# Optimization experiments

Measured on AMD Instinct MI355X. Metric: run time of the kernel, lower is better.

Reference implementation:

```python
import jax, jax.numpy as jnp
import numpy as np

COMMITMENT_COST = 0.25

def setup_inputs() -> dict:
    key = jax.random.key(0)
    k1, k2 = jax.random.split(key)
    inputs = jax.random.normal(k1, (32, 64, 64, 64), dtype=jnp.float32)  # [B, C=D, H, W]
    K, D = 512, 64
    # torch init: uniform(-1/K, 1/K)
    weight = jax.random.uniform(k2, (K, D), dtype=jnp.float32, minval=-1.0 / K, maxval=1.0 / K)
    return {"inputs": inputs, "weight": weight}

def reference(inputs, weight):
    B, C, H, W = inputs.shape
    x = jnp.transpose(inputs, (0, 2, 3, 1))  # [B, H, W, C]
    flat = x.reshape(-1, C)  # [N, D]
    # squared euclidean distances [N, K]
    d = (jnp.sum(flat ** 2, axis=1, keepdims=True)
         + jnp.sum(weight ** 2, axis=1)
         - 2.0 * flat @ weight.T)
    idx = jnp.argmin(d, axis=1)  # [N]
    quantized = weight[idx]  # gather == one-hot @ weight, [N, D]
    e_latent_loss = jnp.mean((jax.lax.stop_gradient(quantized) - flat) ** 2)
    q_latent_loss = jnp.mean((quantized - jax.lax.stop_gradient(flat)) ** 2)
    loss = q_latent_loss + COMMITMENT_COST * e_latent_loss
    # straight-through estimator
    q_st = flat + jax.lax.stop_gradient(quantized - flat)
    out = jnp.transpose(q_st.reshape(B, H, W, C), (0, 3, 1, 2))  # back to NCHW
    return out, loss
```

## Files before the change

### kernel.cpp

```cpp
#include <hip/hip_runtime.h>

typedef __attribute__((ext_vector_type(8))) __bf16 bf16x8;
typedef __attribute__((ext_vector_type(4))) float floatx4;

__device__ __forceinline__ unsigned short f2bf(float f) {
    unsigned int u = __builtin_bit_cast(unsigned int, f);
    unsigned int r = u + 0x7FFFu + ((u >> 16) & 1u);
    return (unsigned short)(r >> 16);
}

__global__ void vq_prep(const float* __restrict__ w, unsigned short* __restrict__ wbf,
                        float* __restrict__ wsq) {
    const int t = threadIdx.x;
    const int row = blockIdx.x * 4 + (t >> 6);
    const int c = t & 63;
    float v = w[row * 64 + c];
    wbf[row * 64 + c] = f2bf(v);
    float s = v * v;
#pragma unroll
    for (int off = 32; off; off >>= 1) s += __shfl_xor(s, off, 64);
    if (c == 0) wsq[row] = s;
}

__global__ void __launch_bounds__(256) vq_main(
    const float* __restrict__ in,
    const float* __restrict__ w,
    const unsigned short* __restrict__ wbf,
    const float* __restrict__ wsq,
    float* __restrict__ out,
    float* __restrict__ partials) {
    __shared__ unsigned short xs[8 * 64 * 8];
    __shared__ float wsqs[512];
    __shared__ float red_s[4][64];
    __shared__ int   red_i[4][64];
    __shared__ int   idx_final[64];
    __shared__ float wave_sum[4];

    const int t = threadIdx.x;
    const int lane = t & 63;
    const int wv = t >> 6;
    const int b = blockIdx.x >> 6;
    const int s0 = (blockIdx.x & 63) << 6;

    const float* in_base = in + ((size_t)b * 64) * 4096 + s0;

    wsqs[t] = wsq[t];
    wsqs[t + 256] = wsq[t + 256];

    const int jj = (t & 15) * 4;
    const int c0 = t >> 4;
#pragma unroll
    for (int co = 0; co < 64; co += 16) {
        const int c = co + c0;
        floatx4 v = *(const floatx4*)(in_base + (size_t)c * 4096 + jj);
        const int g = c >> 3, e = c & 7;
        unsigned short* p = &xs[((g * 64 + jj) * 8) + e];
        p[0]  = f2bf(v[0]);
        p[8]  = f2bf(v[1]);
        p[16] = f2bf(v[2]);
        p[24] = f2bf(v[3]);
    }
    __syncthreads();

    bf16x8 Bf[4][2];
    {
        const int half = lane >> 4;
        const int mcol = lane & 15;
#pragma unroll
        for (int mt = 0; mt < 4; ++mt) {
            const int m = mt * 16 + mcol;
#pragma unroll
            for (int h = 0; h < 2; ++h) {
                const int g = h * 4 + half;
                Bf[mt][h] = *(const bf16x8*)&xs[(g * 64 + m) * 8];
            }
        }
    }

    float best_s[4];
    int   best_i[4];
#pragma unroll
    for (int mt = 0; mt < 4; ++mt) { best_s[mt] = 1e30f; best_i[mt] = 0; }

    const int code_row = lane & 15;
    const int kgrp = lane >> 4;
#pragma unroll
    for (int cti = 0; cti < 8; ++cti) {
        const int ct = wv * 8 + cti;
        const int code_base = ct * 16;
        const unsigned short* arow = wbf + (code_base + code_row) * 64 + kgrp * 8;
        bf16x8 A0 = *(const bf16x8*)(arow);
        bf16x8 A1 = *(const bf16x8*)(arow + 32);
        floatx4 wq = *(const floatx4*)&wsqs[code_base + kgrp * 4];
#pragma unroll
        for (int mt = 0; mt < 4; ++mt) {
            floatx4 acc = {0.f, 0.f, 0.f, 0.f};
            acc = __builtin_amdgcn_mfma_f32_16x16x32_bf16(A0, Bf[mt][0], acc, 0, 0, 0);
            acc = __builtin_amdgcn_mfma_f32_16x16x32_bf16(A1, Bf[mt][1], acc, 0, 0, 0);
#pragma unroll
            for (int r = 0; r < 4; ++r) {
                const float sc = wq[r] - 2.f * acc[r];
                const int code = code_base + kgrp * 4 + r;
                if (sc < best_s[mt]) { best_s[mt] = sc; best_i[mt] = code; }
            }
        }
    }

#pragma unroll
    for (int mt = 0; mt < 4; ++mt) {
        float s = best_s[mt];
        int   i = best_i[mt];
#pragma unroll
        for (int d = 16; d < 64; d <<= 1) {
            const float s2 = __shfl_xor(s, d, 64);
            const int   i2 = __shfl_xor(i, d, 64);
            if (s2 < s || (s2 == s && i2 < i)) { s = s2; i = i2; }
        }
        if (lane < 16) { red_s[wv][mt * 16 + lane] = s; red_i[wv][mt * 16 + lane] = i; }
    }
    __syncthreads();
    if (t < 64) {
        float s = red_s[0][t];
        int   i = red_i[0][t];
#pragma unroll
        for (int w2 = 1; w2 < 4; ++w2) {
            const float s2 = red_s[w2][t];
            const int   i2 = red_i[w2][t];
            if (s2 < s || (s2 == s && i2 < i)) { s = s2; i = i2; }
        }
        idx_final[t] = i;
    }
    __syncthreads();

    int idxr[4];
    idxr[0] = idx_final[jj + 0];
    idxr[1] = idx_final[jj + 1];
    idxr[2] = idx_final[jj + 2];
    idxr[3] = idx_final[jj + 3];

    float lsum = 0.f;
    float* out_base = out + ((size_t)b * 64) * 4096 + s0;
#pragma unroll
    for (int co = 0; co < 64; co += 16) {
        const int c = co + c0;
        floatx4 xv = *(const floatx4*)(in_base + (size_t)c * 4096 + jj);
        floatx4 qv;
#pragma unroll
        for (int r = 0; r < 4; ++r) {
            const float wr = w[idxr[r] * 64 + c];
            qv[r] = wr;
            const float d = wr - xv[r];
            lsum += d * d;
        }
        *(floatx4*)(out_base + (size_t)c * 4096 + jj) = qv;
    }

#pragma unroll
    for (int off = 32; off; off >>= 1) lsum += __shfl_xor(lsum, off, 64);
    if (lane == 0) wave_sum[wv] = lsum;
    __syncthreads();
    if (t == 0) {
        partials[blockIdx.x] = wave_sum[0] + wave_sum[1] + wave_sum[2] + wave_sum[3];
    }
}

__global__ void vq_reduce(const float* __restrict__ partials, float* __restrict__ loss) {
    const int t = threadIdx.x;
    float s = 0.f;
#pragma unroll
    for (int i = 0; i < 8; ++i) s += partials[t + i * 256];
#pragma unroll
    for (int off = 32; off; off >>= 1) s += __shfl_xor(s, off, 64);
    __shared__ float ws4[4];
    if ((t & 63) == 0) ws4[t >> 6] = s;
    __syncthreads();
    if (t == 0) loss[0] = (ws4[0] + ws4[1] + ws4[2] + ws4[3]) * (1.25f / 8388608.f);
}

extern "C" void kernel_launch(void* const* d_in, const int* in_sizes, int n_in,
                              void* d_out, int out_size, void* d_ws, size_t ws_size,
                              hipStream_t stream) {
    const float* in = (const float*)d_in[0];
    const float* w  = (const float*)d_in[1];
    float* out = (float*)d_out;
    float* loss = out + 8388608;
    unsigned short* wbf = (unsigned short*)d_ws;
    float* wsq = (float*)((char*)d_ws + 512 * 64 * 2);
    float* partials = (float*)((char*)d_ws + 512 * 64 * 2 + 2048);

    vq_prep<<<128, 256, 0, stream>>>(w, wbf, wsq);
    vq_main<<<2048, 256, 0, stream>>>(in, w, wbf, wsq, out, partials);
    vq_reduce<<<1, 256, 0, stream>>>(partials, loss);
}
```

Before: 116.4 us.

## Restructure VQ kernel to single-wave blocks with 32x32 MFMA and packed argmin

```diff
diff --git a/kernel.cpp b/kernel.cpp
--- a/kernel.cpp
+++ b/kernel.cpp
@@ -2,6 +2,7 @@
 
 typedef __attribute__((ext_vector_type(8))) __bf16 bf16x8;
 typedef __attribute__((ext_vector_type(4))) float floatx4;
+typedef __attribute__((ext_vector_type(16))) float floatx16;
 
 __device__ __forceinline__ unsigned short f2bf(float f) {
     unsigned int u = __builtin_bit_cast(unsigned int, f);
@@ -22,39 +23,32 @@
     if (c == 0) wsq[row] = s;
 }
 
-__global__ void __launch_bounds__(256) vq_main(
+__global__ void __launch_bounds__(64, 4) vq_main(
     const float* __restrict__ in,
     const float* __restrict__ w,
     const unsigned short* __restrict__ wbf,
     const float* __restrict__ wsq,
     float* __restrict__ out,
     float* __restrict__ partials) {
-    __shared__ unsigned short xs[8 * 64 * 8];
-    __shared__ float wsqs[512];
-    __shared__ float red_s[4][64];
-    __shared__ int   red_i[4][64];
-    __shared__ int   idx_final[64];
-    __shared__ float wave_sum[4];
+    __shared__ unsigned short xs[8 * 32 * 8];
 
-    const int t = threadIdx.x;
-    const int lane = t & 63;
-    const int wv = t >> 6;
-    const int b = blockIdx.x >> 6;
-    const int s0 = (blockIdx.x & 63) << 6;
+    const int lane = threadIdx.x;
+    const int bid = blockIdx.x;
+    const int b = bid >> 7;
+    const int s0 = (bid & 127) << 5;
 
     const float* in_base = in + ((size_t)b * 64) * 4096 + s0;
+    const int c0 = lane >> 3;
+    const int jj = (lane & 7) * 4;
 
-    wsqs[t] = wsq[t];
-    wsqs[t + 256] = wsq[t + 256];
-
-    const int jj = (t & 15) * 4;
-    const int c0 = t >> 4;
+    float x2 = 0.f;
 #pragma unroll
-    for (int co = 0; co < 64; co += 16) {
-        const int c = co + c0;
-        floatx4 v = *(const floatx4*)(in_base + (size_t)c * 4096 + jj);
-        const int g = c >> 3, e = c & 7;
-        unsigned short* p = &xs[((g * 64 + jj) * 8) + e];
+    for (int co = 0; co < 64; co += 8) {
+        const int k = co + c0;
+        floatx4 v = *(const floatx4*)(in_base + (size_t)k * 4096 + jj);
+        x2 += v[0] * v[0] + v[1] * v[1] + v[2] * v[2] + v[3] * v[3];
+        const int g = k >> 3, e = k & 7;
+        unsigned short* p = &xs[(g * 32 + jj) * 8 + e];
         p[0]  = f2bf(v[0]);
         p[8]  = f2bf(v[1]);
         p[16] = f2bf(v[2]);
@@ -62,105 +56,68 @@
     }
     __syncthreads();
 
-    bf16x8 Bf[4][2];
-    {
-        const int half = lane >> 4;
-        const int mcol = lane & 15;
+    const int hi = lane >> 5;
+    const int col = lane & 31;
+
+    bf16x8 Bf[4];
 #pragma unroll
-        for (int mt = 0; mt < 4; ++mt) {
-            const int m = mt * 16 + mcol;
+    for (int ch = 0; ch < 4; ++ch) {
+        const int g = 2 * ch + hi;
+        Bf[ch] = *(const bf16x8*)&xs[(g * 32 + col) * 8];
+    }
+
+    float best = 1e30f;
+#pragma unroll 2
+    for (int ct = 0; ct < 16; ++ct) {
+        const int code_base = ct * 32;
+        const unsigned short* arow = wbf + (code_base + col) * 64 + hi * 8;
+        bf16x8 A0 = *(const bf16x8*)(arow);
+        bf16x8 A1 = *(const bf16x8*)(arow + 16);
+        bf16x8 A2 = *(const bf16x8*)(arow + 32);
+        bf16x8 A3 = *(const bf16x8*)(arow + 48);
+        floatx16 acc = {0.f, 0.f, 0.f, 0.f, 0.f, 0.f, 0.f, 0.f,
+                        0.f, 0.f, 0.f, 0.f, 0.f, 0.f, 0.f, 0.f};
+        acc = __builtin_amdgcn_mfma_f32_32x32x16_bf16(A0, Bf[0], acc, 0, 0, 0);
+        acc = __builtin_amdgcn_mfma_f32_32x32x16_bf16(A1, Bf[1], acc, 0, 0, 0);
+        acc = __builtin_amdgcn_mfma_f32_32x32x16_bf16(A2, Bf[2], acc, 0, 0, 0);
+        acc = __builtin_amdgcn_mfma_f32_32x32x16_bf16(A3, Bf[3], acc, 0, 0, 0);
 #pragma unroll
-            for (int h = 0; h < 2; ++h) {
-                const int g = h * 4 + half;
-                Bf[mt][h] = *(const bf16x8*)&xs[(g * 64 + m) * 8];
+        for (int q = 0; q < 4; ++q) {
+            floatx4 wq = *(const floatx4*)&wsq[code_base + 8 * q + 4 * hi];
+#pragma unroll
+            for (int rr = 0; rr < 4; ++rr) {
+                const int r = q * 4 + rr;
+                const float sc = __builtin_fmaf(-2.f, acc[r], wq[rr]);
+                const unsigned int code = (unsigned int)(code_base + 8 * q + 4 * hi + rr);
+                const unsigned int ub =
+                    (__builtin_bit_cast(unsigned int, sc) & 0xFFFFFE00u) | code;
+                best = fminf(best, __builtin_bit_cast(float, ub));
             }
         }
     }
+    best = fminf(best, __shfl_xor(best, 32, 64));
 
-    float best_s[4];
-    int   best_i[4];
+    const float smin =
+        __builtin_bit_cast(float, __builtin_bit_cast(unsigned int, best) & 0xFFFFFE00u);
+    float tot = x2 + (lane < 32 ? smin : 0.f);
 #pragma unroll
-    for (int mt = 0; mt < 4; ++mt) { best_s[mt] = 1e30f; best_i[mt] = 0; }
-
-    const int code_row = lane & 15;
-    const int kgrp = lane >> 4;
-#pragma unroll
-    for (int cti = 0; cti < 8; ++cti) {
-        const int ct = wv * 8 + cti;
-        const int code_base = ct * 16;
-        const unsigned short* arow = wbf + (code_base + code_row) * 64 + kgrp * 8;
-        bf16x8 A0 = *(const bf16x8*)(arow);
-        bf16x8 A1 = *(const bf16x8*)(arow + 32);
-        floatx4 wq = *(const floatx4*)&wsqs[code_base + kgrp * 4];
-#pragma unroll
-        for (int mt = 0; mt < 4; ++mt) {
-            floatx4 acc = {0.f, 0.f, 0.f, 0.f};
-            acc = __builtin_amdgcn_mfma_f32_16x16x32_bf16(A0, Bf[mt][0], acc, 0, 0, 0);
-            acc = __builtin_amdgcn_mfma_f32_16x16x32_bf16(A1, Bf[mt][1], acc, 0, 0, 0);
-#pragma unroll
-            for (int r = 0; r < 4; ++r) {
-                const float sc = wq[r] - 2.f * acc[r];
-                const int code = code_base + kgrp * 4 + r;
-                if (sc < best_s[mt]) { best_s[mt] = sc; best_i[mt] = code; }
-            }
-        }
-    }
-
-#pragma unroll
-    for (int mt = 0; mt < 4; ++mt) {
-        float s = best_s[mt];
-        int   i = best_i[mt];
-#pragma unroll
-        for (int d = 16; d < 64; d <<= 1) {
-            const float s2 = __shfl_xor(s, d, 64);
-            const int   i2 = __shfl_xor(i, d, 64);
-            if (s2 < s || (s2 == s && i2 < i)) { s = s2; i = i2; }
-        }
-        if (lane < 16) { red_s[wv][mt * 16 + lane] = s; red_i[wv][mt * 16 + lane] = i; }
-    }
-    __syncthreads();
-    if (t < 64) {
-        float s = red_s[0][t];
-        int   i = red_i[0][t];
-#pragma unroll
-        for (int w2 = 1; w2 < 4; ++w2) {
-            const float s2 = red_s[w2][t];
-            const int   i2 = red_i[w2][t];
-            if (s2 < s || (s2 == s && i2 < i)) { s = s2; i = i2; }
-        }
-        idx_final[t] = i;
-    }
-    __syncthreads();
+    for (int off = 1; off < 64; off <<= 1) tot += __shfl_xor(tot, off, 64);
+    if (lane == 0) partials[bid] = tot;
 
     int idxr[4];
-    idxr[0] = idx_final[jj + 0];
-    idxr[1] = idx_final[jj + 1];
-    idxr[2] = idx_final[jj + 2];
-    idxr[3] = idx_final[jj + 3];
-
-    float lsum = 0.f;
+#pragma unroll
+    for (int r = 0; r < 4; ++r) {
+        const float pk = __shfl(best, jj + r, 64);
+        idxr[r] = (int)(__builtin_bit_cast(unsigned int, pk) & 511u);
+    }
     float* out_base = out + ((size_t)b * 64) * 4096 + s0;
 #pragma unroll
-    for (int co = 0; co < 64; co += 16) {
+    for (int co = 0; co < 64; co += 8) {
         const int c = co + c0;
-        floatx4 xv = *(const floatx4*)(in_base + (size_t)c * 4096 + jj);
         floatx4 qv;
 #pragma unroll
-        for (int r = 0; r < 4; ++r) {
-            const float wr = w[idxr[r] * 64 + c];
-            qv[r] = wr;
-            const float d = wr - xv[r];
-            lsum += d * d;
-        }
+        for (int r = 0; r < 4; ++r) qv[r] = w[idxr[r] * 64 + c];
         *(floatx4*)(out_base + (size_t)c * 4096 + jj) = qv;
-    }
-
-#pragma unroll
-    for (int off = 32; off; off >>= 1) lsum += __shfl_xor(lsum, off, 64);
-    if (lane == 0) wave_sum[wv] = lsum;
-    __syncthreads();
-    if (t == 0) {
-        partials[blockIdx.x] = wave_sum[0] + wave_sum[1] + wave_sum[2] + wave_sum[3];
     }
 }
 
@@ -168,7 +125,7 @@
     const int t = threadIdx.x;
     float s = 0.f;
 #pragma unroll
-    for (int i = 0; i < 8; ++i) s += partials[t + i * 256];
+    for (int i = 0; i < 16; ++i) s += partials[t + i * 256];
 #pragma unroll
     for (int off = 32; off; off >>= 1) s += __shfl_xor(s, off, 64);
     __shared__ float ws4[4];
@@ -189,6 +146,6 @@
     float* partials = (float*)((char*)d_ws + 512 * 64 * 2 + 2048);
 
     vq_prep<<<128, 256, 0, stream>>>(w, wbf, wsq);
-    vq_main<<<2048, 256, 0, stream>>>(in, w, wbf, wsq, out, partials);
+    vq_main<<<4096, 64, 0, stream>>>(in, w, wbf, wsq, out, partials);
     vq_reduce<<<1, 256, 0, stream>>>(partials, loss);
 }
```

Measured after the change: 129.1 us. 10.8% more time.
